# Optimization experiments

Measured on AMD Instinct MI355X. Metric: run time of the kernel, lower is better.

## Reference

```python
import jax, jax.numpy as jnp
import numpy as np

B, S, DM, H, NSYN = 4, 2048, 768, 12, 4
HD = DM // H  # 64
EPS = 1e-12
SCALE = float(DM / H) ** -0.5  # 1/sqrt(head_dim)


def setup_inputs() -> dict:
    key = jax.random.key(0)
    ks = jax.random.split(key, 16)
    p = 0.02
    return {
        "hidden_states": jax.random.normal(ks[0], (B, S, DM), jnp.float32),
        "attention_mask": jnp.zeros((B, 1, 1, S), jnp.float32),
        "addi_key": jax.random.normal(ks[1], (B, NSYN, S, HD), jnp.float32),
        "addi_value": jax.random.normal(ks[2], (B, NSYN, S, HD), jnp.float32),
        "Wq": jax.random.normal(ks[3], (DM, DM), jnp.float32) * p,
        "bq": jnp.zeros((DM,), jnp.float32),
        "Wk": jax.random.normal(ks[4], (DM, DM), jnp.float32) * p,
        "bk": jnp.zeros((DM,), jnp.float32),
        "Wv": jax.random.normal(ks[5], (DM, DM), jnp.float32) * p,
        "bv": jnp.zeros((DM,), jnp.float32),
        "Wo": jax.random.normal(ks[6], (DM, DM), jnp.float32) * p,
        "bo": jnp.zeros((DM,), jnp.float32),
        "ln_g": jnp.ones((DM,), jnp.float32),
        "ln_b": jnp.zeros((DM,), jnp.float32),
    }


def _heads(x):
    # [B,S,DM] -> [B,H,S,HD]
    return x.reshape(B, S, H, HD).transpose(0, 2, 1, 3)


def reference(hidden_states, attention_mask, addi_key, addi_value,
              Wq, bq, Wk, bk, Wv, bv, Wo, bo, ln_g, ln_b):
    x = hidden_states
    q = _heads(jnp.einsum('bsi,oi->bso', x, Wq) + bq)
    k = _heads(jnp.einsum('bsi,oi->bso', x, Wk) + bk)
    v = _heads(jnp.einsum('bsi,oi->bso', x, Wv) + bv)
    # additive key/value injection on first NSYN heads
    k = k.at[:, :NSYN].add(addi_key)
    v = v.at[:, :NSYN].add(addi_value)
    scores = jnp.einsum('bhqd,bhkd->bhqk', q, k) * SCALE + attention_mask
    probs = jax.nn.softmax(scores, axis=-1)
    ctx = jnp.einsum('bhqk,bhkd->bhqd', probs, v)
    ctx = ctx.transpose(0, 2, 1, 3).reshape(B, S, DM)
    out = jnp.einsum('bsi,oi->bso', ctx, Wo) + bo
    h = out + x  # residual
    mu = jnp.mean(h, axis=-1, keepdims=True)
    var = jnp.mean((h - mu) ** 2, axis=-1, keepdims=True)
    return (h - mu) * jax.lax.rsqrt(var + EPS) * ln_g + ln_b
```

## Files before the change

kernel.cpp:

```cpp
#include <hip/hip_runtime.h>


typedef __bf16 bf16;
typedef __bf16 bf16x8 __attribute__((ext_vector_type(8)));
typedef __bf16 bf16x4 __attribute__((ext_vector_type(4)));
typedef float floatx4 __attribute__((ext_vector_type(4)));
typedef unsigned int uint2v __attribute__((ext_vector_type(2)));

#define BB 4
#define SS 2048
#define DM 768
#define HH 12
#define HD 64
#define NSYN 4
#define MM (BB*SS)
#define KK DM
#define SCALE 0.125f
#define LOG2E 1.4426950408889634f
#define QSCALE (SCALE * LOG2E)

#define N_X   ((size_t)MM * DM)
#define N_W   ((size_t)DM * DM)
#define N_M   ((size_t)BB * SS)

#if __has_builtin(__builtin_amdgcn_exp2f)
#define EXP2(x) __builtin_amdgcn_exp2f(x)
#else
#define EXP2(x) exp2f(x)
#endif

#define ASYNC16(gp, lp)                                                        \
    __builtin_amdgcn_global_load_lds(                                          \
        (const __attribute__((address_space(1))) unsigned int*)(gp),           \
        (__attribute__((address_space(3))) unsigned int*)(lp), 16, 0, 0)

static __device__ __forceinline__ void pl32_swap(unsigned int& a, unsigned int& b) {
#if __has_builtin(__builtin_amdgcn_permlane32_swap)
    uint2v r = __builtin_amdgcn_permlane32_swap(a, b, false, false);
    a = r[0]; b = r[1];
#else
    asm volatile("v_permlane32_swap_b32 %0, %1" : "+v"(a), "+v"(b));
#endif
}
static __device__ __forceinline__ void pl16_swap(unsigned int& a, unsigned int& b) {
#if __has_builtin(__builtin_amdgcn_permlane16_swap)
    uint2v r = __builtin_amdgcn_permlane16_swap(a, b, false, false);
    a = r[0]; b = r[1];
#else
    asm volatile("v_permlane16_swap_b32 %0, %1" : "+v"(a), "+v"(b));
#endif
}

__global__ __launch_bounds__(256) void cvt_kernel(
    const float* __restrict__ x,
    const float* __restrict__ Wq, const float* __restrict__ Wk,
    const float* __restrict__ Wv, const float* __restrict__ Wo,
    const float* __restrict__ mask,
    bf16* __restrict__ xb,
    bf16* __restrict__ Wqb, bf16* __restrict__ Wkb,
    bf16* __restrict__ Wvb, bf16* __restrict__ Wob,
    float* __restrict__ ml2e)
{
    const size_t nx4 = N_X / 4, nw4 = N_W / 4, nm4 = N_M / 4;
    size_t i = (size_t)blockIdx.x * blockDim.x + threadIdx.x;
    if (i >= nx4 + 4 * nw4) {
        size_t off = i - nx4 - 4 * nw4;
        if (off < nm4) {
            float4 m = *(const float4*)(mask + off * 4);
            float4 o = { m.x * LOG2E, m.y * LOG2E, m.z * LOG2E, m.w * LOG2E };
            *(float4*)(ml2e + off * 4) = o;
        }
        return;
    }
    const float* src; bf16* dst; size_t off;
    if (i < nx4)                { src = x;  dst = xb;  off = i; }
    else if (i < nx4 + nw4)     { src = Wq; dst = Wqb; off = i - nx4; }
    else if (i < nx4 + 2*nw4)   { src = Wk; dst = Wkb; off = i - nx4 - nw4; }
    else if (i < nx4 + 3*nw4)   { src = Wv; dst = Wvb; off = i - nx4 - 2*nw4; }
    else                        { src = Wo; dst = Wob; off = i - nx4 - 3*nw4; }
    float4 v = *(const float4*)(src + off * 4);
    bf16x4 o = { (bf16)v.x, (bf16)v.y, (bf16)v.z, (bf16)v.w };
    *(bf16x4*)(dst + off * 4) = o;
}

#define STG_CL(lane)  (((lane) & 3) ^ (((lane) >> 2) & 3) ^ (((lane) >> 4) & 3))
#define FRG_PC(quad, l15)  ((quad) ^ ((l15) & 3) ^ (((l15) >> 2) & 3))

template<int ORD>
__device__ __forceinline__ void gemm_mainloop64(
    const bf16* __restrict__ A, const bf16* __restrict__ Bw,
    int tileM, int tileN, bf16* As, bf16* Bs, floatx4 acc[2][4])
{
    const int tid  = threadIdx.x;
    const int lane = tid & 63;
    const int wave = tid >> 6;
    const int l15 = lane & 15, quad = lane >> 4;

    const int r0a = wave * 32 + (lane >> 2);
    const int r0b = wave * 16 + (lane >> 2);
    const int cl  = STG_CL(lane);
    const bf16* gA = A  + (size_t)(tileM * 128 + r0a) * KK + cl * 8;
    const bf16* gB = Bw + (size_t)(tileN *  64 + r0b) * KK + cl * 8;
    bf16* lA = As + (wave * 32) * 32;
    bf16* lB = Bs + (wave * 16) * 32;

    ASYNC16(gA,           lA);
    ASYNC16(gA + 16 * KK, lA + 16 * 32);
    ASYNC16(gB,           lB);
    __syncthreads();

    const int fpc = FRG_PC(quad, l15);
    for (int kt = 0; kt < KK / 32; ++kt) {
        const int cur = kt & 1;
        if (kt + 1 < KK / 32) {
            const int nbA = (1 - cur) * 4096;
            const int nbB = (1 - cur) * 2048;
            ASYNC16(gA + (kt + 1) * 32,           lA + nbA);
            ASYNC16(gA + (kt + 1) * 32 + 16 * KK, lA + nbA + 16 * 32);
            ASYNC16(gB + (kt + 1) * 32,           lB + nbB);
        }
        const bf16* cA = As + cur * 4096;
        const bf16* cB = Bs + cur * 2048;
        bf16x8 af[2], bfr[4];
        #pragma unroll
        for (int i = 0; i < 2; ++i)
            af[i] = *(const bf16x8*)(cA + (wave * 32 + i * 16 + l15) * 32 + fpc * 8);
        #pragma unroll
        for (int j = 0; j < 4; ++j)
            bfr[j] = *(const bf16x8*)(cB + (j * 16 + l15) * 32 + fpc * 8);
        #pragma unroll
        for (int i = 0; i < 2; ++i)
            #pragma unroll
            for (int j = 0; j < 4; ++j)
                acc[i][j] = (ORD == 0)
                    ? __builtin_amdgcn_mfma_f32_16x16x32_bf16(af[i], bfr[j], acc[i][j], 0, 0, 0)
                    : __builtin_amdgcn_mfma_f32_16x16x32_bf16(bfr[j], af[i], acc[i][j], 0, 0, 0);
        __syncthreads();
    }
}

template<int ORD>
__device__ __forceinline__ void gemm_mainloop128(
    const bf16* __restrict__ A, const bf16* __restrict__ Bw,
    int tileM, bf16* As, bf16* Bs, floatx4 acc[2][8])
{
    const int tid  = threadIdx.x;
    const int lane = tid & 63;
    const int wave = tid >> 6;
    const int l15 = lane & 15, quad = lane >> 4;

    const int r0 = wave * 32 + (lane >> 2);
    const int cl = STG_CL(lane);
    const bf16* gA = A  + (size_t)(tileM * 128 + r0) * KK + cl * 8;
    const bf16* gB = Bw + (size_t)r0 * KK + cl * 8;
    bf16* lA = As + (wave * 32) * 32;
    bf16* lB = Bs + (wave * 32) * 32;

    ASYNC16(gA,           lA);
    ASYNC16(gA + 16 * KK, lA + 16 * 32);
    ASYNC16(gB,           lB);
    ASYNC16(gB + 16 * KK, lB + 16 * 32);
    __syncthreads();

    const int fpc = FRG_PC(quad, l15);
    for (int kt = 0; kt < KK / 32; ++kt) {
        const int cur = kt & 1;
        if (kt + 1 < KK / 32) {
            const int nb = (1 - cur) * 4096;
            ASYNC16(gA + (kt + 1) * 32,           lA + nb);
            ASYNC16(gA + (kt + 1) * 32 + 16 * KK, lA + nb + 16 * 32);
            ASYNC16(gB + (kt + 1) * 32,           lB + nb);
            ASYNC16(gB + (kt + 1) * 32 + 16 * KK, lB + nb + 16 * 32);
        }
        const bf16* cA = As + cur * 4096;
        const bf16* cB = Bs + cur * 4096;
        bf16x8 af[2];
        #pragma unroll
        for (int i = 0; i < 2; ++i)
            af[i] = *(const bf16x8*)(cA + (wave * 32 + i * 16 + l15) * 32 + fpc * 8);
        #pragma unroll
        for (int j = 0; j < 8; ++j) {
            bf16x8 bfr = *(const bf16x8*)(cB + (j * 16 + l15) * 32 + fpc * 8);
            #pragma unroll
            for (int i = 0; i < 2; ++i)
                acc[i][j] = (ORD == 0)
                    ? __builtin_amdgcn_mfma_f32_16x16x32_bf16(af[i], bfr, acc[i][j], 0, 0, 0)
                    : __builtin_amdgcn_mfma_f32_16x16x32_bf16(bfr, af[i], acc[i][j], 0, 0, 0);
        }
        __syncthreads();
    }
}

__global__ __launch_bounds__(256, 4) void qkv_kernel(
    const bf16* __restrict__ xb,
    const bf16* __restrict__ Wqb, const float* __restrict__ bq,
    const bf16* __restrict__ Wkb, const float* __restrict__ bk,
    const bf16* __restrict__ Wvb, const float* __restrict__ bv,
    const float* __restrict__ addi_key, const float* __restrict__ addi_value,
    bf16* __restrict__ qbuf, bf16* __restrict__ kbuf, bf16* __restrict__ vtbuf)
{
    __shared__ __align__(16) bf16 As[2 * 128 * 32];
    __shared__ __align__(16) bf16 Bs[2 * 128 * 32];
    const int u = blockIdx.x;
    const int tileM = u & 63;
    const int tileN = u >> 6;
    const int z     = tileN / 6;
    const int tN    = tileN % 6;
    const bf16* W     = (z == 0) ? Wqb : (z == 1) ? Wkb : Wvb;
    const float* bias = (z == 0) ? bq  : (z == 1) ? bk  : bv;
    const bf16* Wrow  = W + (size_t)(tN * 128) * KK;

    floatx4 acc[2][8];
    #pragma unroll
    for (int i = 0; i < 2; ++i)
        #pragma unroll
        for (int j = 0; j < 8; ++j) { floatx4 zv = {0.f, 0.f, 0.f, 0.f}; acc[i][j] = zv; }

    const int lane = threadIdx.x & 63, wave = threadIdx.x >> 6;
    const int l15 = lane & 15, quad = lane >> 4;

    if (z == 2) {
        gemm_mainloop128<0>(xb, Wrow, tileM, As, Bs, acc);
        #pragma unroll
        for (int i = 0; i < 2; ++i) {
            const int sg0 = tileM * 128 + wave * 32 + i * 16 + quad * 4;
            const int b = sg0 >> 11, s0 = sg0 & 2047;
            #pragma unroll
            for (int j = 0; j < 8; ++j) {
                const int o = tN * 128 + j * 16 + l15;
                const float bv_ = bias[o];
                const int h = o >> 6, d = o & 63;
                float vv[4];
                #pragma unroll
                for (int rr = 0; rr < 4; ++rr) {
                    vv[rr] = acc[i][j][rr] + bv_;
                    if (h < NSYN)
                        vv[rr] += addi_value[(((size_t)b * NSYN + h) * SS + s0 + rr) * HD + d];
                }
                bf16x4 pk = { (bf16)vv[0], (bf16)vv[1], (bf16)vv[2], (bf16)vv[3] };
                *(bf16x4*)(vtbuf + (((size_t)b * HH + h) * HD + d) * SS + s0) = pk;
            }
        }
    } else {
        gemm_mainloop128<1>(xb, Wrow, tileM, As, Bs, acc);
        #pragma unroll
        for (int i = 0; i < 2; ++i) {
            const int sg = tileM * 128 + wave * 32 + i * 16 + l15;
            const int b = sg >> 11, s = sg & 2047;
            #pragma unroll
            for (int j = 0; j < 8; ++j) {
                const int o0 = tN * 128 + j * 16 + quad * 4;
                const int h = o0 >> 6, d0 = o0 & 63;
                float4 b4 = *(const float4*)(bias + o0);
                float vv[4] = { acc[i][j][0] + b4.x, acc[i][j][1] + b4.y,
                                acc[i][j][2] + b4.z, acc[i][j][3] + b4.w };
                if (z == 1 && h < NSYN) {
                    float4 a4 = *(const float4*)(addi_key +
                        (((size_t)b * NSYN + h) * SS + s) * HD + d0);
                    vv[0] += a4.x; vv[1] += a4.y; vv[2] += a4.z; vv[3] += a4.w;
                }
                if (z == 0) {
                    bf16x4 pk = { (bf16)(vv[0] * QSCALE), (bf16)(vv[1] * QSCALE),
                                  (bf16)(vv[2] * QSCALE), (bf16)(vv[3] * QSCALE) };
                    *(bf16x4*)(qbuf + (((size_t)b * HH + h) * SS + s) * HD + d0) = pk;
                } else {
                    bf16x4 pk = { (bf16)vv[0], (bf16)vv[1], (bf16)vv[2], (bf16)vv[3] };
                    *(bf16x4*)(kbuf + (((size_t)b * HH + h) * SS + s) * HD + d0) = pk;
                }
            }
        }
    }
}

__global__ __launch_bounds__(256, 3) void attn_kernel(
    const bf16* __restrict__ qbuf, const bf16* __restrict__ kbuf,
    const bf16* __restrict__ vtbuf, const float* __restrict__ ml2e,
    bf16* __restrict__ ctx)
{
    __shared__ __align__(16) bf16 Ks[2 * 64 * 64];
    __shared__ __align__(16) bf16 Vt[2 * 64 * 64];

    const int u  = blockIdx.x;
    const int bh = u % 48;
    const int qt = u / 48;
    const int b  = bh / 12;
    const int h  = bh % 12;
    const size_t bhs = ((size_t)b * HH + h) * SS * HD;
    const int tid = threadIdx.x, lane = tid & 63, wave = tid >> 6;
    const int l15 = lane & 15, quad = lane >> 4;
    const int q0 = qt * 128 + wave * 32;

    const int sr  = wave * 16 + (lane >> 3);
    const int scl = (lane & 7) ^ ((lane >> 3) & 7);
    const bf16* gK = kbuf  + bhs + (size_t)sr * HD + scl * 8;
    const bf16* gV = vtbuf + bhs + (size_t)sr * SS + scl * 8;
    bf16* lK = Ks + (wave * 16) * 64;
    bf16* lV = Vt + (wave * 16) * 64;

    bf16x8 qf[2][2];
    #pragma unroll
    for (int n = 0; n < 2; ++n)
        #pragma unroll
        for (int c = 0; c < 2; ++c)
            qf[n][c] = *(const bf16x8*)(qbuf + bhs +
                (size_t)(q0 + n * 16 + l15) * HD + c * 32 + quad * 8);

    bf16x8 ones;
    #pragma unroll
    for (int e = 0; e < 8; ++e) ones[e] = (bf16)1.0f;

    floatx4 acco[2][4];
    #pragma unroll
    for (int n = 0; n < 2; ++n)
        #pragma unroll
        for (int t = 0; t < 4; ++t) { floatx4 zv = {0.f, 0.f, 0.f, 0.f}; acco[n][t] = zv; }
    floatx4 lacc[2];
    { floatx4 zv = {0.f, 0.f, 0.f, 0.f}; lacc[0] = zv; lacc[1] = zv; }

    const float* mb = ml2e + (size_t)b * SS;

    #pragma unroll
    for (int p = 0; p < 2; ++p) {
        ASYNC16(gK + (size_t)p * 8 * HD,  lK + p * 512);
        ASYNC16(gV + (size_t)p * 8 * SS,  lV + p * 512);
    }
    __syncthreads();

    for (int kt = 0; kt < SS / 64; ++kt) {
        const int cur = kt & 1;
        if (kt + 1 < SS / 64) {
            const int nb = (1 - cur) * 4096;
            #pragma unroll
            for (int p = 0; p < 2; ++p) {
                ASYNC16(gK + ((size_t)(kt + 1) * 64 + p * 8) * HD, lK + nb + p * 512);
                ASYNC16(gV + (size_t)p * 8 * SS + (kt + 1) * 64,   lV + nb + p * 512);
            }
        }
        const bf16* cK = Ks + cur * 4096;
        const bf16* cV = Vt + cur * 4096;

        floatx4 sacc[2][4];
        #pragma unroll
        for (int j = 0; j < 4; ++j) {
            float4 mk = *(const float4*)(mb + kt * 64 + j * 16 + quad * 4);
            floatx4 mv = { mk.x, mk.y, mk.z, mk.w };
            sacc[0][j] = mv;
            sacc[1][j] = mv;
        }
        __builtin_amdgcn_s_setprio(1);
        #pragma unroll
        for (int c = 0; c < 2; ++c) {
            const int pc = (4 * c + quad) ^ (l15 & 7);
            #pragma unroll
            for (int j = 0; j < 4; ++j) {
                bf16x8 af = *(const bf16x8*)(cK + (j * 16 + l15) * 64 + pc * 8);
                #pragma unroll
                for (int n = 0; n < 2; ++n)
                    sacc[n][j] = __builtin_amdgcn_mfma_f32_16x16x32_bf16(af, qf[n][c], sacc[n][j], 0, 0, 0);
            }
        }
        __builtin_amdgcn_s_setprio(0);

        unsigned int w[2][4][2];
        #pragma unroll
        for (int j = 0; j < 4; ++j) {
            #pragma unroll
            for (int n = 0; n < 2; ++n) {
                float p0 = EXP2(sacc[n][j][0]);
                float p1 = EXP2(sacc[n][j][1]);
                float p2 = EXP2(sacc[n][j][2]);
                float p3 = EXP2(sacc[n][j][3]);
                union { bf16x4 v; unsigned int u2[2]; } pk;
                pk.v = (bf16x4){ (bf16)p0, (bf16)p1, (bf16)p2, (bf16)p3 };
                w[n][j][0] = pk.u2[0];
                w[n][j][1] = pk.u2[1];
            }
        }
        #pragma unroll
        for (int n = 0; n < 2; ++n) {
            pl32_swap(w[n][0][0], w[n][1][0]);  pl32_swap(w[n][0][1], w[n][1][1]);
            pl32_swap(w[n][2][0], w[n][3][0]);  pl32_swap(w[n][2][1], w[n][3][1]);
        }
        #pragma unroll
        for (int n = 0; n < 2; ++n) {
            pl16_swap(w[n][0][0], w[n][1][0]);  pl16_swap(w[n][0][1], w[n][1][1]);
            pl16_swap(w[n][2][0], w[n][3][0]);  pl16_swap(w[n][2][1], w[n][3][1]);
        }
        union { unsigned int u2[4]; bf16x8 v; } pb[2][2];
        #pragma unroll
        for (int n = 0; n < 2; ++n) {
            pb[n][0].u2[0] = w[n][0][0]; pb[n][0].u2[1] = w[n][0][1];
            pb[n][0].u2[2] = w[n][1][0]; pb[n][0].u2[3] = w[n][1][1];
            pb[n][1].u2[0] = w[n][2][0]; pb[n][1].u2[1] = w[n][2][1];
            pb[n][1].u2[2] = w[n][3][0]; pb[n][1].u2[3] = w[n][3][1];
        }

        __builtin_amdgcn_s_setprio(1);
        #pragma unroll
        for (int c = 0; c < 2; ++c) {
            const int pc = (4 * c + quad) ^ (l15 & 7);
            #pragma unroll
            for (int n = 0; n < 2; ++n)
                lacc[n] = __builtin_amdgcn_mfma_f32_16x16x32_bf16(ones, pb[n][c].v, lacc[n], 0, 0, 0);
            #pragma unroll
            for (int t = 0; t < 4; ++t) {
                bf16x8 af = *(const bf16x8*)(cV + (t * 16 + l15) * 64 + pc * 8);
                #pragma unroll
                for (int n = 0; n < 2; ++n)
                    acco[n][t] = __builtin_amdgcn_mfma_f32_16x16x32_bf16(af, pb[n][c].v, acco[n][t], 0, 0, 0);
            }
        }
        __builtin_amdgcn_s_setprio(0);
        __syncthreads();
    }

    #pragma unroll
    for (int n = 0; n < 2; ++n) {
        const float inv = 1.0f / lacc[n][0];
        bf16* crow = ctx + ((size_t)(b * SS + q0 + n * 16 + l15)) * DM + h * HD;
        #pragma unroll
        for (int t = 0; t < 4; ++t) {
            bf16x4 ov = { (bf16)(acco[n][t][0] * inv), (bf16)(acco[n][t][1] * inv),
                          (bf16)(acco[n][t][2] * inv), (bf16)(acco[n][t][3] * inv) };
            *(bf16x4*)(crow + t * 16 + quad * 4) = ov;
        }
    }
}

__global__ __launch_bounds__(256) void oproj_kernel(
    const bf16* __restrict__ ctx, const bf16* __restrict__ Wob,
    const float* __restrict__ bo, const float* __restrict__ x,
    bf16* __restrict__ hbuf)
{
    __shared__ __align__(16) bf16 As[2 * 128 * 32];
    __shared__ __align__(16) bf16 Bs[2 * 64 * 32];
    const int u = blockIdx.x;
    const int tileM = u & 63;
    const int tileN = u >> 6;

    floatx4 acc[2][4];
    #pragma unroll
    for (int i = 0; i < 2; ++i)
        #pragma unroll
        for (int j = 0; j < 4; ++j) { floatx4 zv = {0.f, 0.f, 0.f, 0.f}; acc[i][j] = zv; }

    gemm_mainloop64<1>(ctx, Wob, tileM, tileN, As, Bs, acc);

    const int lane = threadIdx.x & 63, wave = threadIdx.x >> 6;
    const int l15 = lane & 15, quad = lane >> 4;
    #pragma unroll
    for (int i = 0; i < 2; ++i) {
        const int sg = tileM * 128 + wave * 32 + i * 16 + l15;
        #pragma unroll
        for (int j = 0; j < 4; ++j) {
            const int o0 = tileN * 64 + j * 16 + quad * 4;
            float4 b4 = *(const float4*)(bo + o0);
            float4 r4 = *(const float4*)(x + (size_t)sg * DM + o0);
            bf16x4 pk = { (bf16)(acc[i][j][0] + b4.x + r4.x),
                          (bf16)(acc[i][j][1] + b4.y + r4.y),
                          (bf16)(acc[i][j][2] + b4.z + r4.z),
                          (bf16)(acc[i][j][3] + b4.w + r4.w) };
            *(bf16x4*)(hbuf + (size_t)sg * DM + o0) = pk;
        }
    }
}

__global__ __launch_bounds__(256) void ln_kernel(
    const bf16* __restrict__ hbuf, const float* __restrict__ g,
    const float* __restrict__ be, float* __restrict__ out)
{
    const int row  = blockIdx.x * 4 + (threadIdx.x >> 6);
    const int lane = threadIdx.x & 63;
    const bf16* hr = hbuf + (size_t)row * DM;

    bf16x8 va = *(const bf16x8*)(hr + lane * 8);
    bf16x4 vb = *(const bf16x4*)(hr + 512 + lane * 4);
    float v[12];
    #pragma unroll
    for (int i = 0; i < 8; ++i) v[i] = (float)va[i];
    #pragma unroll
    for (int i = 0; i < 4; ++i) v[8 + i] = (float)vb[i];

    float s = 0.f;
    #pragma unroll
    for (int i = 0; i < 12; ++i) s += v[i];
    #pragma unroll
    for (int m = 1; m < 64; m <<= 1) s += __shfl_xor(s, m);
    const float mu = s * (1.0f / DM);

    float s2 = 0.f;
    #pragma unroll
    for (int i = 0; i < 12; ++i) { v[i] -= mu; s2 += v[i] * v[i]; }
    #pragma unroll
    for (int m = 1; m < 64; m <<= 1) s2 += __shfl_xor(s2, m);
    const float rsv = rsqrtf(s2 * (1.0f / DM) + 1e-12f);

    float* orow = out + (size_t)row * DM;
    const int c0 = lane * 8, c1 = 512 + lane * 4;
    float4 g0 = *(const float4*)(g + c0),     g1 = *(const float4*)(g + c0 + 4);
    float4 g2 = *(const float4*)(g + c1);
    float4 b0 = *(const float4*)(be + c0),    b1 = *(const float4*)(be + c0 + 4);
    float4 b2 = *(const float4*)(be + c1);
    float4 o0 = { v[0]*rsv*g0.x + b0.x, v[1]*rsv*g0.y + b0.y,
                  v[2]*rsv*g0.z + b0.z, v[3]*rsv*g0.w + b0.w };
    float4 o1 = { v[4]*rsv*g1.x + b1.x, v[5]*rsv*g1.y + b1.y,
                  v[6]*rsv*g1.z + b1.z, v[7]*rsv*g1.w + b1.w };
    float4 o2 = { v[8]*rsv*g2.x + b2.x, v[9]*rsv*g2.y + b2.y,
                  v[10]*rsv*g2.z + b2.z, v[11]*rsv*g2.w + b2.w };
    *(float4*)(orow + c0)     = o0;
    *(float4*)(orow + c0 + 4) = o1;
    *(float4*)(orow + c1)     = o2;
}

extern "C" void kernel_launch(void* const* d_in, const int* in_sizes, int n_in,
                              void* d_out, int out_size, void* d_ws, size_t ws_size,
                              hipStream_t stream)
{
    const float* x    = (const float*)d_in[0];
    const float* mask = (const float*)d_in[1];
    const float* akey = (const float*)d_in[2];
    const float* aval = (const float*)d_in[3];
    const float* Wq = (const float*)d_in[4];  const float* bq = (const float*)d_in[5];
    const float* Wk = (const float*)d_in[6];  const float* bk = (const float*)d_in[7];
    const float* Wv = (const float*)d_in[8];  const float* bv = (const float*)d_in[9];
    const float* Wo = (const float*)d_in[10]; const float* bo = (const float*)d_in[11];
    const float* lng = (const float*)d_in[12]; const float* lnb = (const float*)d_in[13];
    float* outp = (float*)d_out;

    const size_t nqkv = (size_t)BB * HH * SS * HD;
    char* ws = (char*)d_ws;
    bf16*  xb   = (bf16*)ws;   ws += N_X  * sizeof(bf16);
    bf16*  Wqb  = (bf16*)ws;   ws += N_W  * sizeof(bf16);
    bf16*  Wkb  = (bf16*)ws;   ws += N_W  * sizeof(bf16);
    bf16*  Wvb  = (bf16*)ws;   ws += N_W  * sizeof(bf16);
    bf16*  Wob  = (bf16*)ws;   ws += N_W  * sizeof(bf16);
    float* ml2e = (float*)ws;  ws += N_M  * sizeof(float);
    bf16*  qbuf = (bf16*)ws;   ws += nqkv * sizeof(bf16);
    bf16*  kbuf = (bf16*)ws;   ws += nqkv * sizeof(bf16);
    bf16*  vtbuf= (bf16*)ws;   ws += nqkv * sizeof(bf16);
    bf16*  ctxb = (bf16*)ws;   ws += nqkv * sizeof(bf16);
    bf16*  hbuf = (bf16*)ws;   ws += nqkv * sizeof(bf16);

    const size_t ncvt = (N_X + 4 * N_W + N_M) / 4;
    const int cvt_blocks = (int)((ncvt + 255) / 256);
    cvt_kernel<<<cvt_blocks, 256, 0, stream>>>(x, Wq, Wk, Wv, Wo, mask,
                                               xb, Wqb, Wkb, Wvb, Wob, ml2e);

    qkv_kernel<<<1152, 256, 0, stream>>>(xb, Wqb, bq, Wkb, bk, Wvb, bv, akey, aval,
                                         qbuf, kbuf, vtbuf);
    attn_kernel<<<768, 256, 0, stream>>>(qbuf, kbuf, vtbuf, ml2e, ctxb);
    oproj_kernel<<<768, 256, 0, stream>>>(ctxb, Wob, bo, x, hbuf);
    ln_kernel<<<MM / 4, 256, 0, stream>>>(hbuf, lng, lnb, outp);
}
```

Before: 268.8 us.

## Triple-buffer GEMM mainloops with single barrier and explicit vmcnt waits

```diff
diff --git a/kernel.cpp b/kernel.cpp
--- a/kernel.cpp
+++ b/kernel.cpp
@@ -86,8 +86,71 @@
 #define STG_CL(lane)  (((lane) & 3) ^ (((lane) >> 2) & 3) ^ (((lane) >> 4) & 3))
 #define FRG_PC(quad, l15)  ((quad) ^ ((l15) & 3) ^ (((l15) >> 2) & 3))
 
+#define PIPE_BARRIER()                                                         \
+    __builtin_amdgcn_sched_barrier(0);                                         \
+    __builtin_amdgcn_s_barrier();                                              \
+    __builtin_amdgcn_sched_barrier(0)
+
 template<int ORD>
-__device__ __forceinline__ void gemm_mainloop64(
+__device__ __forceinline__ void gemm_mainloop128p(
+    const bf16* __restrict__ A, const bf16* __restrict__ Bw,
+    int tileM, bf16* As, bf16* Bs, floatx4 acc[2][8])
+{
+    const int tid  = threadIdx.x;
+    const int lane = tid & 63;
+    const int wave = tid >> 6;
+    const int l15 = lane & 15, quad = lane >> 4;
+
+    const int r0 = wave * 32 + (lane >> 2);
+    const int cl = STG_CL(lane);
+    const bf16* gA = A  + (size_t)(tileM * 128 + r0) * KK + cl * 8;
+    const bf16* gB = Bw + (size_t)r0 * KK + cl * 8;
+    bf16* lA = As + (wave * 32) * 32;
+    bf16* lB = Bs + (wave * 32) * 32;
+
+    ASYNC16(gA,                lA);
+    ASYNC16(gA + 16 * KK,      lA + 512);
+    ASYNC16(gB,                lB);
+    ASYNC16(gB + 16 * KK,      lB + 512);
+    ASYNC16(gA + 32,           lA + 4096);
+    ASYNC16(gA + 32 + 16 * KK, lA + 4096 + 512);
+    ASYNC16(gB + 32,           lB + 4096);
+    ASYNC16(gB + 32 + 16 * KK, lB + 4096 + 512);
+
+    const int fpc = FRG_PC(quad, l15);
+    int bo = 0;
+    for (int kt = 0; kt < KK / 32; ++kt) {
+        if (kt + 1 < KK / 32) asm volatile("s_waitcnt vmcnt(4)" ::: "memory");
+        else                  asm volatile("s_waitcnt vmcnt(0)" ::: "memory");
+        PIPE_BARRIER();
+        if (kt + 2 < KK / 32) {
+            int nb = bo + 8192; if (nb >= 12288) nb -= 12288;
+            ASYNC16(gA + (kt + 2) * 32,           lA + nb);
+            ASYNC16(gA + (kt + 2) * 32 + 16 * KK, lA + nb + 512);
+            ASYNC16(gB + (kt + 2) * 32,           lB + nb);
+            ASYNC16(gB + (kt + 2) * 32 + 16 * KK, lB + nb + 512);
+        }
+        const bf16* cA = As + bo;
+        const bf16* cB = Bs + bo;
+        bf16x8 af[2];
+        #pragma unroll
+        for (int i = 0; i < 2; ++i)
+            af[i] = *(const bf16x8*)(cA + (wave * 32 + i * 16 + l15) * 32 + fpc * 8);
+        #pragma unroll
+        for (int j = 0; j < 8; ++j) {
+            bf16x8 bfr = *(const bf16x8*)(cB + (j * 16 + l15) * 32 + fpc * 8);
+            #pragma unroll
+            for (int i = 0; i < 2; ++i)
+                acc[i][j] = (ORD == 0)
+                    ? __builtin_amdgcn_mfma_f32_16x16x32_bf16(af[i], bfr, acc[i][j], 0, 0, 0)
+                    : __builtin_amdgcn_mfma_f32_16x16x32_bf16(bfr, af[i], acc[i][j], 0, 0, 0);
+        }
+        bo += 4096; if (bo == 12288) bo = 0;
+    }
+}
+
+template<int ORD>
+__device__ __forceinline__ void gemm_mainloop64p(
     const bf16* __restrict__ A, const bf16* __restrict__ Bw,
     int tileM, int tileN, bf16* As, bf16* Bs, floatx4 acc[2][4])
 {
@@ -104,23 +167,28 @@
     bf16* lA = As + (wave * 32) * 32;
     bf16* lB = Bs + (wave * 16) * 32;
 
-    ASYNC16(gA,           lA);
-    ASYNC16(gA + 16 * KK, lA + 16 * 32);
-    ASYNC16(gB,           lB);
-    __syncthreads();
+    ASYNC16(gA,                lA);
+    ASYNC16(gA + 16 * KK,      lA + 512);
+    ASYNC16(gB,                lB);
+    ASYNC16(gA + 32,           lA + 4096);
+    ASYNC16(gA + 32 + 16 * KK, lA + 4096 + 512);
+    ASYNC16(gB + 32,           lB + 2048);
 
     const int fpc = FRG_PC(quad, l15);
+    int boA = 0, boB = 0;
     for (int kt = 0; kt < KK / 32; ++kt) {
-        const int cur = kt & 1;
-        if (kt + 1 < KK / 32) {
-            const int nbA = (1 - cur) * 4096;
-            const int nbB = (1 - cur) * 2048;
-            ASYNC16(gA + (kt + 1) * 32,           lA + nbA);
-            ASYNC16(gA + (kt + 1) * 32 + 16 * KK, lA + nbA + 16 * 32);
-            ASYNC16(gB + (kt + 1) * 32,           lB + nbB);
-        }
-        const bf16* cA = As + cur * 4096;
-        const bf16* cB = Bs + cur * 2048;
+        if (kt + 1 < KK / 32) asm volatile("s_waitcnt vmcnt(3)" ::: "memory");
+        else                  asm volatile("s_waitcnt vmcnt(0)" ::: "memory");
+        PIPE_BARRIER();
+        if (kt + 2 < KK / 32) {
+            int nA = boA + 8192; if (nA >= 12288) nA -= 12288;
+            int nB = boB + 4096; if (nB >=  6144) nB -=  6144;
+            ASYNC16(gA + (kt + 2) * 32,           lA + nA);
+            ASYNC16(gA + (kt + 2) * 32 + 16 * KK, lA + nA + 512);
+            ASYNC16(gB + (kt + 2) * 32,           lB + nB);
+        }
+        const bf16* cA = As + boA;
+        const bf16* cB = Bs + boB;
         bf16x8 af[2], bfr[4];
         #pragma unroll
         for (int i = 0; i < 2; ++i)
@@ -135,63 +203,12 @@
                 acc[i][j] = (ORD == 0)
                     ? __builtin_amdgcn_mfma_f32_16x16x32_bf16(af[i], bfr[j], acc[i][j], 0, 0, 0)
                     : __builtin_amdgcn_mfma_f32_16x16x32_bf16(bfr[j], af[i], acc[i][j], 0, 0, 0);
-        __syncthreads();
-    }
-}
-
-template<int ORD>
-__device__ __forceinline__ void gemm_mainloop128(
-    const bf16* __restrict__ A, const bf16* __restrict__ Bw,
-    int tileM, bf16* As, bf16* Bs, floatx4 acc[2][8])
-{
-    const int tid  = threadIdx.x;
-    const int lane = tid & 63;
-    const int wave = tid >> 6;
-    const int l15 = lane & 15, quad = lane >> 4;
-
-    const int r0 = wave * 32 + (lane >> 2);
-    const int cl = STG_CL(lane);
-    const bf16* gA = A  + (size_t)(tileM * 128 + r0) * KK + cl * 8;
-    const bf16* gB = Bw + (size_t)r0 * KK + cl * 8;
-    bf16* lA = As + (wave * 32) * 32;
-    bf16* lB = Bs + (wave * 32) * 32;
-
-    ASYNC16(gA,           lA);
-    ASYNC16(gA + 16 * KK, lA + 16 * 32);
-    ASYNC16(gB,           lB);
-    ASYNC16(gB + 16 * KK, lB + 16 * 32);
-    __syncthreads();
-
-    const int fpc = FRG_PC(quad, l15);
-    for (int kt = 0; kt < KK / 32; ++kt) {
-        const int cur = kt & 1;
-        if (kt + 1 < KK / 32) {
-            const int nb = (1 - cur) * 4096;
-            ASYNC16(gA + (kt + 1) * 32,           lA + nb);
-            ASYNC16(gA + (kt + 1) * 32 + 16 * KK, lA + nb + 16 * 32);
-            ASYNC16(gB + (kt + 1) * 32,           lB + nb);
-            ASYNC16(gB + (kt + 1) * 32 + 16 * KK, lB + nb + 16 * 32);
-        }
-        const bf16* cA = As + cur * 4096;
-        const bf16* cB = Bs + cur * 4096;
-        bf16x8 af[2];
-        #pragma unroll
-        for (int i = 0; i < 2; ++i)
-            af[i] = *(const bf16x8*)(cA + (wave * 32 + i * 16 + l15) * 32 + fpc * 8);
-        #pragma unroll
-        for (int j = 0; j < 8; ++j) {
-            bf16x8 bfr = *(const bf16x8*)(cB + (j * 16 + l15) * 32 + fpc * 8);
-            #pragma unroll
-            for (int i = 0; i < 2; ++i)
-                acc[i][j] = (ORD == 0)
-                    ? __builtin_amdgcn_mfma_f32_16x16x32_bf16(af[i], bfr, acc[i][j], 0, 0, 0)
-                    : __builtin_amdgcn_mfma_f32_16x16x32_bf16(bfr, af[i], acc[i][j], 0, 0, 0);
-        }
-        __syncthreads();
-    }
-}
-
-__global__ __launch_bounds__(256, 4) void qkv_kernel(
+        boA += 4096; if (boA == 12288) boA = 0;
+        boB += 2048; if (boB ==  6144) boB = 0;
+    }
+}
+
+__global__ __launch_bounds__(256, 3) void qkv_kernel(
     const bf16* __restrict__ xb,
     const bf16* __restrict__ Wqb, const float* __restrict__ bq,
     const bf16* __restrict__ Wkb, const float* __restrict__ bk,
@@ -199,8 +216,8 @@
     const float* __restrict__ addi_key, const float* __restrict__ addi_value,
     bf16* __restrict__ qbuf, bf16* __restrict__ kbuf, bf16* __restrict__ vtbuf)
 {
-    __shared__ __align__(16) bf16 As[2 * 128 * 32];
-    __shared__ __align__(16) bf16 Bs[2 * 128 * 32];
+    __shared__ __align__(16) bf16 As[3 * 128 * 32];
+    __shared__ __align__(16) bf16 Bs[3 * 128 * 32];
     const int u = blockIdx.x;
     const int tileM = u & 63;
     const int tileN = u >> 6;
@@ -220,7 +237,7 @@
     const int l15 = lane & 15, quad = lane >> 4;
 
     if (z == 2) {
-        gemm_mainloop128<0>(xb, Wrow, tileM, As, Bs, acc);
+        gemm_mainloop128p<0>(xb, Wrow, tileM, As, Bs, acc);
         #pragma unroll
         for (int i = 0; i < 2; ++i) {
             const int sg0 = tileM * 128 + wave * 32 + i * 16 + quad * 4;
@@ -242,7 +259,7 @@
             }
         }
     } else {
-        gemm_mainloop128<1>(xb, Wrow, tileM, As, Bs, acc);
+        gemm_mainloop128p<1>(xb, Wrow, tileM, As, Bs, acc);
         #pragma unroll
         for (int i = 0; i < 2; ++i) {
             const int sg = tileM * 128 + wave * 32 + i * 16 + l15;
@@ -327,6 +344,11 @@
     __syncthreads();
 
     for (int kt = 0; kt < SS / 64; ++kt) {
+        float4 mk4[4];
+        #pragma unroll
+        for (int j = 0; j < 4; ++j)
+            mk4[j] = *(const float4*)(mb + kt * 64 + j * 16 + quad * 4);
+
         const int cur = kt & 1;
         if (kt + 1 < SS / 64) {
             const int nb = (1 - cur) * 4096;
@@ -342,8 +364,7 @@
         floatx4 sacc[2][4];
         #pragma unroll
         for (int j = 0; j < 4; ++j) {
-            float4 mk = *(const float4*)(mb + kt * 64 + j * 16 + quad * 4);
-            floatx4 mv = { mk.x, mk.y, mk.z, mk.w };
+            floatx4 mv = { mk4[j].x, mk4[j].y, mk4[j].z, mk4[j].w };
             sacc[0][j] = mv;
             sacc[1][j] = mv;
         }
@@ -427,13 +448,13 @@
     }
 }
 
-__global__ __launch_bounds__(256) void oproj_kernel(
+__global__ __launch_bounds__(256, 3) void oproj_kernel(
     const bf16* __restrict__ ctx, const bf16* __restrict__ Wob,
     const float* __restrict__ bo, const float* __restrict__ x,
     bf16* __restrict__ hbuf)
 {
-    __shared__ __align__(16) bf16 As[2 * 128 * 32];
-    __shared__ __align__(16) bf16 Bs[2 * 64 * 32];
+    __shared__ __align__(16) bf16 As[3 * 128 * 32];
+    __shared__ __align__(16) bf16 Bs[3 * 64 * 32];
     const int u = blockIdx.x;
     const int tileM = u & 63;
     const int tileN = u >> 6;
@@ -444,7 +465,7 @@
         #pragma unroll
         for (int j = 0; j < 4; ++j) { floatx4 zv = {0.f, 0.f, 0.f, 0.f}; acc[i][j] = zv; }
 
-    gemm_mainloop64<1>(ctx, Wob, tileM, tileN, As, Bs, acc);
+    gemm_mainloop64p<1>(ctx, Wob, tileM, tileN, As, Bs, acc);
 
     const int lane = threadIdx.x & 63, wave = threadIdx.x >> 6;
     const int l15 = lane & 15, quad = lane >> 4;
```

New measurement: 277.3 us. 3.2% more time.
